# Performance work log

Hardware: AMD Instinct MI355X
Metric: run time of the kernel (lower is better)

Reference implementation:

```python
import jax, jax.numpy as jnp
import numpy as np

N = 12288       # number of edge-triangle incidences
D_IN = 2        # input_dim
D_K = 8         # d_k
H1 = 32
H2 = 16
N_EDGES = 6144  # number of segments for scatter_softmax
N_TRI = 4096


def _layernorm(x, g, b, eps=1e-5):
    mu = jnp.mean(x, axis=-1, keepdims=True)
    var = jnp.mean((x - mu) ** 2, axis=-1, keepdims=True)
    return (x - mu) / jnp.sqrt(var + eps) * g + b


def _rmsnorm(x, w, eps=1e-6):
    rms = jnp.sqrt(jnp.mean(x ** 2, axis=-1, keepdims=True))
    return x / (rms + eps) * w


def setup_inputs() -> dict:
    key = jax.random.key(0)
    ks = jax.random.split(key, 16)

    def lin(k, out_d, in_d):
        k1, k2 = jax.random.split(k)
        bound = 1.0 / np.sqrt(in_d)
        W = jax.random.uniform(k1, (out_d, in_d), jnp.float32, -bound, bound)
        b = jax.random.uniform(k2, (out_d,), jnp.float32, -bound, bound)
        return W, b

    Wq, bq = lin(ks[0], D_K, D_IN)
    Wk, bk = lin(ks[1], D_K, D_IN)
    Wv, bv = lin(ks[2], D_K, D_IN)
    W1, b1 = lin(ks[3], H1, D_K)    # Linear(d_k, 32)
    Wr, br = lin(ks[4], H1, H1)     # ResBlock Linear(32, 32)
    W2, b2 = lin(ks[5], H2, H1)     # Linear(32, 16)
    W3, b3 = lin(ks[6], 1, H2)      # Linear(16, 1)

    return {
        "edge_features": jax.random.normal(ks[7], (N, D_IN), jnp.float32),
        "edge_ids_all": jax.random.randint(ks[8], (N,), 0, N_EDGES, jnp.int32),
        "triangle_ids_all": jax.random.randint(ks[9], (N,), 0, N_TRI, jnp.int32),
        "Wq": Wq, "bq": bq, "Wk": Wk, "bk": bk, "Wv": Wv, "bv": bv,
        "W1": W1, "b1": b1,
        "ln1_g": jnp.ones((H1,), jnp.float32), "ln1_b": jnp.zeros((H1,), jnp.float32),
        "rms_w": jnp.ones((H1,), jnp.float32),
        "Wr": Wr, "br": br,
        "ln2_g": jnp.ones((H1,), jnp.float32), "ln2_b": jnp.zeros((H1,), jnp.float32),
        "W2": W2, "b2": b2, "W3": W3, "b3": b3,
    }


def reference(edge_features, edge_ids_all, triangle_ids_all,
              Wq, bq, Wk, bk, Wv, bv,
              W1, b1, ln1_g, ln1_b, rms_w, Wr, br, ln2_g, ln2_b,
              W2, b2, W3, b3):
    q = edge_features @ Wq.T + bq          # [N, d_k]
    k = edge_features @ Wk.T + bk
    v = edge_features @ Wv.T + bv

    scores = (q @ k.T) / np.sqrt(D_K).astype(np.float32)   # [N, N]
    mask = triangle_ids_all[:, None] == triangle_ids_all[None, :]
    scores = jnp.where(mask, scores, -jnp.inf)
    attn = jax.nn.softmax(scores, axis=1)                   # row softmax
    attended = attn @ v                                     # [N, d_k]

    # attention_mlp
    h = _layernorm(attended @ W1.T + b1, ln1_g, ln1_b)
    h = jax.nn.gelu(h, approximate=False)
    h = h + jax.nn.relu(_rmsnorm(h, rms_w) @ Wr.T + br)     # ResBlock
    h = _layernorm(h, ln2_g, ln2_b)
    h = jax.nn.gelu(h @ W2.T + b2, approximate=False)
    logits = (h @ W3.T + b3)[:, 0]                          # [N]

    # scatter_softmax over edge_ids segments
    seg_max = jax.ops.segment_max(logits, edge_ids_all, num_segments=N_EDGES)
    seg_max = jnp.where(jnp.isfinite(seg_max), seg_max, 0.0)
    e = jnp.exp(logits - seg_max[edge_ids_all])
    seg_sum = jax.ops.segment_sum(e, edge_ids_all, num_segments=N_EDGES)
    weights = e / seg_sum[edge_ids_all]
    return weights
```

## Files before the change

### kernel.cpp

```cpp
#include <hip/hip_runtime.h>
#include <math.h>

#define N_INC   12288
#define N_EDGES 6144
#define N_TRI   4096
#define CAP_T   32
#define CAP_E   16

__device__ __forceinline__ float gelu_exact(float x) {
    return 0.5f * x * (1.0f + erff(x * 0.70710678118654752f));
}

__global__ void __launch_bounds__(256) k_qkv_fill(
    const float* __restrict__ ef, const int* __restrict__ eid, const int* __restrict__ tri,
    const float* __restrict__ Wq, const float* __restrict__ bq,
    const float* __restrict__ Wk, const float* __restrict__ bk,
    const float* __restrict__ Wv, const float* __restrict__ bv,
    float* __restrict__ q, float* __restrict__ k, float* __restrict__ v,
    int* __restrict__ tri_cnt, int* __restrict__ tri_bkt,
    int* __restrict__ edge_cnt, int* __restrict__ edge_bkt)
{
    int i = blockIdx.x * 256 + threadIdx.x;
    if (i >= N_INC) return;
    float2 x = ((const float2*)ef)[i];
    float qq[8], kk[8], vv[8];
#pragma unroll
    for (int d = 0; d < 8; d++) {
        qq[d] = fmaf(Wq[d*2], x.x, fmaf(Wq[d*2+1], x.y, bq[d]));
        kk[d] = fmaf(Wk[d*2], x.x, fmaf(Wk[d*2+1], x.y, bk[d]));
        vv[d] = fmaf(Wv[d*2], x.x, fmaf(Wv[d*2+1], x.y, bv[d]));
    }
    ((float4*)q)[i*2+0] = make_float4(qq[0],qq[1],qq[2],qq[3]);
    ((float4*)q)[i*2+1] = make_float4(qq[4],qq[5],qq[6],qq[7]);
    ((float4*)k)[i*2+0] = make_float4(kk[0],kk[1],kk[2],kk[3]);
    ((float4*)k)[i*2+1] = make_float4(kk[4],kk[5],kk[6],kk[7]);
    ((float4*)v)[i*2+0] = make_float4(vv[0],vv[1],vv[2],vv[3]);
    ((float4*)v)[i*2+1] = make_float4(vv[4],vv[5],vv[6],vv[7]);

    int t = tri[i];
    int s = atomicAdd(&tri_cnt[t], 1);
    if (s < CAP_T) tri_bkt[t * CAP_T + s] = i;
    int e = eid[i];
    s = atomicAdd(&edge_cnt[e], 1);
    if (s < CAP_E) edge_bkt[e * CAP_E + s] = i;
}

__global__ void __launch_bounds__(256) k_main(
    const float* __restrict__ q, const float* __restrict__ kbuf, const float* __restrict__ vbuf,
    const int* __restrict__ tri, const int* __restrict__ tri_cnt, const int* __restrict__ tri_bkt,
    const float* __restrict__ W1, const float* __restrict__ b1,
    const float* __restrict__ ln1g, const float* __restrict__ ln1b,
    const float* __restrict__ rmsw,
    const float* __restrict__ Wr, const float* __restrict__ br,
    const float* __restrict__ ln2g, const float* __restrict__ ln2b,
    const float* __restrict__ W2, const float* __restrict__ b2,
    const float* __restrict__ W3, const float* __restrict__ b3,
    float* __restrict__ logits)
{
    __shared__ float sW1[256], sb1[32], sg1[32], sB1[32], srw[32];
    __shared__ float sWr[1024], sbr[32], sg2[32], sB2[32];
    __shared__ float sW2[512], sb2[16], sW3[16];

    const int tid = threadIdx.x;
#define CP(dst, src, len) for (int x_ = tid; x_ < (len); x_ += 256) dst[x_] = src[x_];
    CP(sW1, W1, 256) CP(sb1, b1, 32) CP(sg1, ln1g, 32) CP(sB1, ln1b, 32) CP(srw, rmsw, 32)
    CP(sWr, Wr, 1024) CP(sbr, br, 32) CP(sg2, ln2g, 32) CP(sB2, ln2b, 32)
    CP(sW2, W2, 512) CP(sb2, b2, 16) CP(sW3, W3, 16)
#undef CP
    __syncthreads();

    int i = blockIdx.x * 256 + tid;
    if (i >= N_INC) return;

    float qi[8];
    {
        float4 qa = ((const float4*)q)[i*2+0];
        float4 qb = ((const float4*)q)[i*2+1];
        qi[0]=qa.x; qi[1]=qa.y; qi[2]=qa.z; qi[3]=qa.w;
        qi[4]=qb.x; qi[5]=qb.y; qi[6]=qb.z; qi[7]=qb.w;
    }

    int t = tri[i];
    int n = min(tri_cnt[t], CAP_T);
    const int* bkt = tri_bkt + t * CAP_T;

    float m = -1e30f, l = 0.f, acc[8];
#pragma unroll
    for (int d = 0; d < 8; d++) acc[d] = 0.f;

    for (int p0 = 0; p0 < n; p0 += 4) {
        int4 jv = *(const int4*)(bkt + p0);
        int jj[4] = { jv.x, jv.y, jv.z, jv.w };
        int j0 = jv.x;
        float sc[4], vl[4][8];
#pragma unroll
        for (int u = 0; u < 4; u++) {
            int j = (p0 + u < n) ? jj[u] : j0;
            float4 ka = ((const float4*)(kbuf + j*8))[0];
            float4 kb = ((const float4*)(kbuf + j*8))[1];
            float s8 = qi[0]*ka.x + qi[1]*ka.y + qi[2]*ka.z + qi[3]*ka.w
                     + qi[4]*kb.x + qi[5]*kb.y + qi[6]*kb.z + qi[7]*kb.w;
            sc[u] = (p0 + u < n) ? s8 * 0.35355339059327373f : -1e30f;
            float4 va = ((const float4*)(vbuf + j*8))[0];
            float4 vb = ((const float4*)(vbuf + j*8))[1];
            vl[u][0]=va.x; vl[u][1]=va.y; vl[u][2]=va.z; vl[u][3]=va.w;
            vl[u][4]=vb.x; vl[u][5]=vb.y; vl[u][6]=vb.z; vl[u][7]=vb.w;
        }
        float cm = fmaxf(fmaxf(sc[0], sc[1]), fmaxf(sc[2], sc[3]));
        float w0 = expf(sc[0]-cm), w1 = expf(sc[1]-cm);
        float w2 = expf(sc[2]-cm), w3 = expf(sc[3]-cm);
        float cl = w0 + w1 + w2 + w3;
        float nm = fmaxf(m, cm);
        float sa = expf(m - nm), sb = expf(cm - nm);
        l = l * sa + cl * sb;
#pragma unroll
        for (int d = 0; d < 8; d++)
            acc[d] = acc[d]*sa + sb*(w0*vl[0][d] + w1*vl[1][d] + w2*vl[2][d] + w3*vl[3][d]);
        m = nm;
    }
    float inv_l = 1.f / l;
    float att[8];
#pragma unroll
    for (int d = 0; d < 8; d++) att[d] = acc[d] * inv_l;

    float h[32];
#pragma unroll
    for (int o = 0; o < 32; o++) {
        float a = sb1[o];
#pragma unroll
        for (int d = 0; d < 8; d++) a += sW1[o*8+d] * att[d];
        h[o] = a;
    }
    {
        float mu = 0.f;
#pragma unroll
        for (int o = 0; o < 32; o++) mu += h[o];
        mu *= (1.f/32.f);
        float var = 0.f;
#pragma unroll
        for (int o = 0; o < 32; o++) { float d = h[o]-mu; var += d*d; }
        var *= (1.f/32.f);
        float is = 1.f / sqrtf(var + 1e-5f);
#pragma unroll
        for (int o = 0; o < 32; o++) h[o] = (h[o]-mu)*is*sg1[o] + sB1[o];
    }
#pragma unroll
    for (int o = 0; o < 32; o++) h[o] = gelu_exact(h[o]);
    {
        float ss = 0.f;
#pragma unroll
        for (int o = 0; o < 32; o++) ss += h[o]*h[o];
        float rms = sqrtf(ss * (1.f/32.f));
        float ir = 1.f / (rms + 1e-6f);
        float hn[32];
#pragma unroll
        for (int o = 0; o < 32; o++) hn[o] = h[o]*ir*srw[o];
#pragma unroll
        for (int o = 0; o < 32; o++) {
            float a = sbr[o];
#pragma unroll
            for (int in = 0; in < 32; in++) a += sWr[o*32+in] * hn[in];
            h[o] += fmaxf(a, 0.f);
        }
    }
    {
        float mu = 0.f;
#pragma unroll
        for (int o = 0; o < 32; o++) mu += h[o];
        mu *= (1.f/32.f);
        float var = 0.f;
#pragma unroll
        for (int o = 0; o < 32; o++) { float d = h[o]-mu; var += d*d; }
        var *= (1.f/32.f);
        float is = 1.f / sqrtf(var + 1e-5f);
#pragma unroll
        for (int o = 0; o < 32; o++) h[o] = (h[o]-mu)*is*sg2[o] + sB2[o];
    }
    float h2[16];
#pragma unroll
    for (int o = 0; o < 16; o++) {
        float a = sb2[o];
#pragma unroll
        for (int in = 0; in < 32; in++) a += sW2[o*32+in] * h[in];
        h2[o] = gelu_exact(a);
    }
    float lg = b3[0];
#pragma unroll
    for (int in = 0; in < 16; in++) lg += sW3[in] * h2[in];

    logits[i] = lg;
}

__global__ void __launch_bounds__(256) k_edge_softmax(
    const float* __restrict__ logits, const int* __restrict__ edge_cnt,
    const int* __restrict__ edge_bkt, float* __restrict__ out)
{
    int e = blockIdx.x * 256 + threadIdx.x;
    if (e >= N_EDGES) return;
    int n = min(edge_cnt[e], CAP_E);
    if (n == 0) return;
    const int4* bp = (const int4*)(edge_bkt + e * CAP_E);
    int4 b0 = bp[0], b1 = bp[1], b2 = bp[2], b3 = bp[3];
    int idx[16] = { b0.x,b0.y,b0.z,b0.w, b1.x,b1.y,b1.z,b1.w,
                    b2.x,b2.y,b2.z,b2.w, b3.x,b3.y,b3.z,b3.w };
    int i0 = b0.x;
    float lg[16];
#pragma unroll
    for (int u = 0; u < 16; u++) {
        int j = (u < n) ? idx[u] : i0;
        float val = logits[j];
        lg[u] = (u < n) ? val : -1e30f;
    }
    float mx = -1e30f;
#pragma unroll
    for (int u = 0; u < 16; u++) mx = fmaxf(mx, lg[u]);
    float ex[16], sum = 0.f;
#pragma unroll
    for (int u = 0; u < 16; u++) { ex[u] = expf(lg[u] - mx); sum += ex[u]; }
    float inv = 1.f / sum;
#pragma unroll
    for (int u = 0; u < 16; u++) if (u < n) out[idx[u]] = ex[u] * inv;
}

extern "C" void kernel_launch(void* const* d_in, const int* in_sizes, int n_in,
                              void* d_out, int out_size, void* d_ws, size_t ws_size,
                              hipStream_t stream) {
    const float* ef   = (const float*)d_in[0];
    const int*   eid  = (const int*)d_in[1];
    const int*   tri  = (const int*)d_in[2];
    const float* Wq   = (const float*)d_in[3];  const float* bq = (const float*)d_in[4];
    const float* Wk   = (const float*)d_in[5];  const float* bk = (const float*)d_in[6];
    const float* Wv   = (const float*)d_in[7];  const float* bv = (const float*)d_in[8];
    const float* W1   = (const float*)d_in[9];  const float* b1 = (const float*)d_in[10];
    const float* ln1g = (const float*)d_in[11]; const float* ln1b = (const float*)d_in[12];
    const float* rmsw = (const float*)d_in[13];
    const float* Wr   = (const float*)d_in[14]; const float* br = (const float*)d_in[15];
    const float* ln2g = (const float*)d_in[16]; const float* ln2b = (const float*)d_in[17];
    const float* W2   = (const float*)d_in[18]; const float* b2 = (const float*)d_in[19];
    const float* W3   = (const float*)d_in[20]; const float* b3 = (const float*)d_in[21];

    float* ws   = (float*)d_ws;
    float* kbuf = ws;
    float* vbuf = kbuf + N_INC*8;
    float* qbuf = vbuf + N_INC*8;
    float* logits = qbuf + N_INC*8;
    int* tri_cnt  = (int*)(logits + N_INC);
    int* edge_cnt = tri_cnt + N_TRI;
    int* tri_bkt  = edge_cnt + N_EDGES;
    int* edge_bkt = tri_bkt + N_TRI*CAP_T;

    hipMemsetAsync(tri_cnt, 0, (size_t)(N_TRI + N_EDGES) * sizeof(int), stream);

    k_qkv_fill<<<48, 256, 0, stream>>>(ef, eid, tri, Wq, bq, Wk, bk, Wv, bv,
                                       qbuf, kbuf, vbuf,
                                       tri_cnt, tri_bkt, edge_cnt, edge_bkt);
    k_main<<<48, 256, 0, stream>>>(qbuf, kbuf, vbuf, tri, tri_cnt, tri_bkt,
                                   W1, b1, ln1g, ln1b, rmsw, Wr, br, ln2g, ln2b,
                                   W2, b2, W3, b3, logits);
    k_edge_softmax<<<24, 256, 0, stream>>>(logits, edge_cnt, edge_bkt, (float*)d_out);
}
```

Measured before the change: 129.8 us.

## Split per-row MLP across four lanes and compute q inline

The attention MLP stage now uses four threads per incidence row, each owning eight hidden features. LayerNorm and RMSNorm statistics and the matvec inputs are exchanged with wavefront shuffles, and the grid grows from 48 to 192 blocks to raise occupancy and cut per-thread register pressure. The q projection is recomputed in the main kernel from the input features instead of being written to and read from a workspace buffer. The attention loop is now done redundantly by all four lanes, and the bounds checks are removed on the assumption that sizes divide exactly.

```diff
diff --git a/kernel.cpp b/kernel.cpp
--- a/kernel.cpp
+++ b/kernel.cpp
@@ -13,25 +13,20 @@
 
 __global__ void __launch_bounds__(256) k_qkv_fill(
     const float* __restrict__ ef, const int* __restrict__ eid, const int* __restrict__ tri,
-    const float* __restrict__ Wq, const float* __restrict__ bq,
     const float* __restrict__ Wk, const float* __restrict__ bk,
     const float* __restrict__ Wv, const float* __restrict__ bv,
-    float* __restrict__ q, float* __restrict__ k, float* __restrict__ v,
+    float* __restrict__ k, float* __restrict__ v,
     int* __restrict__ tri_cnt, int* __restrict__ tri_bkt,
     int* __restrict__ edge_cnt, int* __restrict__ edge_bkt)
 {
     int i = blockIdx.x * 256 + threadIdx.x;
-    if (i >= N_INC) return;
     float2 x = ((const float2*)ef)[i];
-    float qq[8], kk[8], vv[8];
+    float kk[8], vv[8];
 #pragma unroll
     for (int d = 0; d < 8; d++) {
-        qq[d] = fmaf(Wq[d*2], x.x, fmaf(Wq[d*2+1], x.y, bq[d]));
         kk[d] = fmaf(Wk[d*2], x.x, fmaf(Wk[d*2+1], x.y, bk[d]));
         vv[d] = fmaf(Wv[d*2], x.x, fmaf(Wv[d*2+1], x.y, bv[d]));
     }
-    ((float4*)q)[i*2+0] = make_float4(qq[0],qq[1],qq[2],qq[3]);
-    ((float4*)q)[i*2+1] = make_float4(qq[4],qq[5],qq[6],qq[7]);
     ((float4*)k)[i*2+0] = make_float4(kk[0],kk[1],kk[2],kk[3]);
     ((float4*)k)[i*2+1] = make_float4(kk[4],kk[5],kk[6],kk[7]);
     ((float4*)v)[i*2+0] = make_float4(vv[0],vv[1],vv[2],vv[3]);
@@ -46,8 +41,10 @@
 }
 
 __global__ void __launch_bounds__(256) k_main(
-    const float* __restrict__ q, const float* __restrict__ kbuf, const float* __restrict__ vbuf,
+    const float* __restrict__ ef,
+    const float* __restrict__ kbuf, const float* __restrict__ vbuf,
     const int* __restrict__ tri, const int* __restrict__ tri_cnt, const int* __restrict__ tri_bkt,
+    const float* __restrict__ Wq, const float* __restrict__ bq,
     const float* __restrict__ W1, const float* __restrict__ b1,
     const float* __restrict__ ln1g, const float* __restrict__ ln1b,
     const float* __restrict__ rmsw,
@@ -69,16 +66,16 @@
 #undef CP
     __syncthreads();
 
-    int i = blockIdx.x * 256 + tid;
-    if (i >= N_INC) return;
-
+    const int g4 = blockIdx.x * 256 + tid;
+    const int i  = g4 >> 2;
+    const int lq = tid & 3;
+    const int ob = lq * 8;
+
+    float2 x = ((const float2*)ef)[i];
     float qi[8];
-    {
-        float4 qa = ((const float4*)q)[i*2+0];
-        float4 qb = ((const float4*)q)[i*2+1];
-        qi[0]=qa.x; qi[1]=qa.y; qi[2]=qa.z; qi[3]=qa.w;
-        qi[4]=qb.x; qi[5]=qb.y; qi[6]=qb.z; qi[7]=qb.w;
-    }
+#pragma unroll
+    for (int d = 0; d < 8; d++)
+        qi[d] = fmaf(Wq[d*2], x.x, fmaf(Wq[d*2+1], x.y, bq[d]));
 
     int t = tri[i];
     int n = min(tri_cnt[t], CAP_T);
@@ -123,72 +120,95 @@
 #pragma unroll
     for (int d = 0; d < 8; d++) att[d] = acc[d] * inv_l;
 
-    float h[32];
-#pragma unroll
-    for (int o = 0; o < 32; o++) {
-        float a = sb1[o];
-#pragma unroll
-        for (int d = 0; d < 8; d++) a += sW1[o*8+d] * att[d];
-        h[o] = a;
+    float h[8];
+#pragma unroll
+    for (int oo = 0; oo < 8; oo++) {
+        float a = sb1[ob+oo];
+#pragma unroll
+        for (int d = 0; d < 8; d++) a += sW1[(ob+oo)*8+d] * att[d];
+        h[oo] = a;
     }
     {
-        float mu = 0.f;
-#pragma unroll
-        for (int o = 0; o < 32; o++) mu += h[o];
-        mu *= (1.f/32.f);
-        float var = 0.f;
-#pragma unroll
-        for (int o = 0; o < 32; o++) { float d = h[o]-mu; var += d*d; }
-        var *= (1.f/32.f);
-        float is = 1.f / sqrtf(var + 1e-5f);
-#pragma unroll
-        for (int o = 0; o < 32; o++) h[o] = (h[o]-mu)*is*sg1[o] + sB1[o];
-    }
-#pragma unroll
-    for (int o = 0; o < 32; o++) h[o] = gelu_exact(h[o]);
+        float s = 0.f;
+#pragma unroll
+        for (int oo = 0; oo < 8; oo++) s += h[oo];
+        s += __shfl_xor(s, 1); s += __shfl_xor(s, 2);
+        float mu = s * (1.f/32.f);
+        float vs = 0.f;
+#pragma unroll
+        for (int oo = 0; oo < 8; oo++) { float d = h[oo]-mu; vs += d*d; }
+        vs += __shfl_xor(vs, 1); vs += __shfl_xor(vs, 2);
+        float is = 1.f / sqrtf(vs * (1.f/32.f) + 1e-5f);
+#pragma unroll
+        for (int oo = 0; oo < 8; oo++) h[oo] = (h[oo]-mu)*is*sg1[ob+oo] + sB1[ob+oo];
+    }
+#pragma unroll
+    for (int oo = 0; oo < 8; oo++) h[oo] = gelu_exact(h[oo]);
+
     {
         float ss = 0.f;
 #pragma unroll
-        for (int o = 0; o < 32; o++) ss += h[o]*h[o];
+        for (int oo = 0; oo < 8; oo++) ss += h[oo]*h[oo];
+        ss += __shfl_xor(ss, 1); ss += __shfl_xor(ss, 2);
         float rms = sqrtf(ss * (1.f/32.f));
         float ir = 1.f / (rms + 1e-6f);
-        float hn[32];
-#pragma unroll
-        for (int o = 0; o < 32; o++) hn[o] = h[o]*ir*srw[o];
-#pragma unroll
-        for (int o = 0; o < 32; o++) {
-            float a = sbr[o];
-#pragma unroll
-            for (int in = 0; in < 32; in++) a += sWr[o*32+in] * hn[in];
-            h[o] += fmaxf(a, 0.f);
+        float hn[8];
+#pragma unroll
+        for (int oo = 0; oo < 8; oo++) hn[oo] = h[oo]*ir*srw[ob+oo];
+        float a[8];
+#pragma unroll
+        for (int oo = 0; oo < 8; oo++) a[oo] = sbr[ob+oo];
+#pragma unroll
+        for (int r = 0; r < 4; r++) {
+            float g[8];
+#pragma unroll
+            for (int s8 = 0; s8 < 8; s8++) g[s8] = __shfl(hn[s8], r, 4);
+#pragma unroll
+            for (int oo = 0; oo < 8; oo++)
+#pragma unroll
+                for (int s8 = 0; s8 < 8; s8++)
+                    a[oo] += sWr[(ob+oo)*32 + r*8 + s8] * g[s8];
         }
+#pragma unroll
+        for (int oo = 0; oo < 8; oo++) h[oo] += fmaxf(a[oo], 0.f);
     }
     {
-        float mu = 0.f;
-#pragma unroll
-        for (int o = 0; o < 32; o++) mu += h[o];
-        mu *= (1.f/32.f);
-        float var = 0.f;
-#pragma unroll
-        for (int o = 0; o < 32; o++) { float d = h[o]-mu; var += d*d; }
-        var *= (1.f/32.f);
-        float is = 1.f / sqrtf(var + 1e-5f);
-#pragma unroll
-        for (int o = 0; o < 32; o++) h[o] = (h[o]-mu)*is*sg2[o] + sB2[o];
-    }
-    float h2[16];
-#pragma unroll
-    for (int o = 0; o < 16; o++) {
-        float a = sb2[o];
-#pragma unroll
-        for (int in = 0; in < 32; in++) a += sW2[o*32+in] * h[in];
-        h2[o] = gelu_exact(a);
-    }
-    float lg = b3[0];
-#pragma unroll
-    for (int in = 0; in < 16; in++) lg += sW3[in] * h2[in];
-
-    logits[i] = lg;
+        float s = 0.f;
+#pragma unroll
+        for (int oo = 0; oo < 8; oo++) s += h[oo];
+        s += __shfl_xor(s, 1); s += __shfl_xor(s, 2);
+        float mu = s * (1.f/32.f);
+        float vs = 0.f;
+#pragma unroll
+        for (int oo = 0; oo < 8; oo++) { float d = h[oo]-mu; vs += d*d; }
+        vs += __shfl_xor(vs, 1); vs += __shfl_xor(vs, 2);
+        float is = 1.f / sqrtf(vs * (1.f/32.f) + 1e-5f);
+#pragma unroll
+        for (int oo = 0; oo < 8; oo++) h[oo] = (h[oo]-mu)*is*sg2[ob+oo] + sB2[ob+oo];
+    }
+    float a2[4];
+#pragma unroll
+    for (int j = 0; j < 4; j++) a2[j] = sb2[lq*4+j];
+#pragma unroll
+    for (int r = 0; r < 4; r++) {
+        float g[8];
+#pragma unroll
+        for (int s8 = 0; s8 < 8; s8++) g[s8] = __shfl(h[s8], r, 4);
+#pragma unroll
+        for (int j = 0; j < 4; j++)
+#pragma unroll
+            for (int s8 = 0; s8 < 8; s8++)
+                a2[j] += sW2[(lq*4+j)*32 + r*8 + s8] * g[s8];
+    }
+    float h2[4];
+#pragma unroll
+    for (int j = 0; j < 4; j++) h2[j] = gelu_exact(a2[j]);
+
+    float lgp = 0.f;
+#pragma unroll
+    for (int j = 0; j < 4; j++) lgp += sW3[lq*4+j] * h2[j];
+    lgp += __shfl_xor(lgp, 1); lgp += __shfl_xor(lgp, 2);
+    if (lq == 0) logits[i] = lgp + b3[0];
 }
 
 __global__ void __launch_bounds__(256) k_edge_softmax(
@@ -196,7 +216,6 @@
     const int* __restrict__ edge_bkt, float* __restrict__ out)
 {
     int e = blockIdx.x * 256 + threadIdx.x;
-    if (e >= N_EDGES) return;
     int n = min(edge_cnt[e], CAP_E);
     if (n == 0) return;
     const int4* bp = (const int4*)(edge_bkt + e * CAP_E);
@@ -242,8 +261,7 @@
     float* ws   = (float*)d_ws;
     float* kbuf = ws;
     float* vbuf = kbuf + N_INC*8;
-    float* qbuf = vbuf + N_INC*8;
-    float* logits = qbuf + N_INC*8;
+    float* logits = vbuf + N_INC*8;
     int* tri_cnt  = (int*)(logits + N_INC);
     int* edge_cnt = tri_cnt + N_TRI;
     int* tri_bkt  = edge_cnt + N_EDGES;
@@ -251,11 +269,11 @@
 
     hipMemsetAsync(tri_cnt, 0, (size_t)(N_TRI + N_EDGES) * sizeof(int), stream);
 
-    k_qkv_fill<<<48, 256, 0, stream>>>(ef, eid, tri, Wq, bq, Wk, bk, Wv, bv,
-                                       qbuf, kbuf, vbuf,
+    k_qkv_fill<<<48, 256, 0, stream>>>(ef, eid, tri, Wk, bk, Wv, bv,
+                                       kbuf, vbuf,
                                        tri_cnt, tri_bkt, edge_cnt, edge_bkt);
-    k_main<<<48, 256, 0, stream>>>(qbuf, kbuf, vbuf, tri, tri_cnt, tri_bkt,
-                                   W1, b1, ln1g, ln1b, rmsw, Wr, br, ln2g, ln2b,
-                                   W2, b2, W3, b3, logits);
+    k_main<<<192, 256, 0, stream>>>(ef, kbuf, vbuf, tri, tri_cnt, tri_bkt,
+                                    Wq, bq, W1, b1, ln1g, ln1b, rmsw, Wr, br,
+                                    ln2g, ln2b, W2, b2, W3, b3, logits);
     k_edge_softmax<<<24, 256, 0, stream>>>(logits, edge_cnt, edge_bkt, (float*)d_out);
 }
```

After: 116.9 us. -9.9%, faster.
